# Optimization experiments

Hardware: AMD Instinct MI355X
Metric: run time of the kernel (lower is better)

The kernel has to match this reference:

```python
import jax, jax.numpy as jnp
import numpy as np

B, S, E, H = 2, 2048, 1024, 8
DH = E // H          # v head dim = 128
F = DH // 2          # q/k sub-head dim = 64


def setup_inputs() -> dict:
    key = jax.random.key(0)
    ks = jax.random.split(key, 7)
    sc = E ** -0.5
    return {
        "x": jax.random.normal(ks[0], (B, S, E), dtype=jnp.float32),
        "Wq": jax.random.normal(ks[1], (E, E), dtype=jnp.float32) * sc,
        "Wk": jax.random.normal(ks[2], (E, E), dtype=jnp.float32) * sc,
        "Wv": jax.random.normal(ks[3], (E, E), dtype=jnp.float32) * sc,
        "norm_w": jnp.ones((H, DH), dtype=jnp.float32),
        "Wo": jax.random.normal(ks[4], (E, E), dtype=jnp.float32) * sc,
        "bo": jnp.zeros((E,), dtype=jnp.float32),
        "diff_weight": jnp.float32(0.2),
    }


def reference(x, Wq, Wk, Wv, norm_w, Wo, bo, diff_weight):
    b, s, e = x.shape
    # projections (Linear with weight [out,in] -> x @ W.T)
    qs = (x @ Wq.T).reshape(b, s, H, 2, F)
    ks_ = (x @ Wk.T).reshape(b, s, H, 2, F)
    vs = (x @ Wv.T).reshape(b, s, H, DH)
    scale = F ** -0.5
    # two attention branches: [2, b, h, q, k]
    scores = jnp.einsum('bqhif,bkhif->ibhqk', qs, ks_) * scale
    atts = jax.nn.softmax(scores, axis=-1)
    att = atts[0] - diff_weight * atts[1]          # [b,h,q,k]
    o = jnp.einsum('bhqk,bkhe->bqhe', att, vs)     # [b,q,h,dh]
    # RMSNorm over the joint (heads, head_dim) dims, as in nn.RMSNorm([H, DH])
    eps = jnp.finfo(o.dtype).eps
    rms = jax.lax.rsqrt(jnp.mean(o * o, axis=(-2, -1), keepdims=True) + eps)
    normed = (o * rms * norm_w).reshape(b, s, e)
    return (normed @ Wo.T + bo) * (1.0 - diff_weight)
```

## Files before the change

kernel.cpp:

```cpp
#include <hip/hip_runtime.h>
#include <hip/hip_bf16.h>
#include <math.h>


#define SDIM 2048
#define EDIM 1024
#define HDIM 8
#define DHDIM 128

typedef unsigned short u16;
typedef __attribute__((ext_vector_type(8))) short bf16x8;
typedef __attribute__((ext_vector_type(4))) short bf16x4;
typedef __attribute__((ext_vector_type(4))) u16 u16x4;
typedef __attribute__((ext_vector_type(8))) u16 u16x8;
typedef __attribute__((ext_vector_type(4))) float f32x4;

__device__ __forceinline__ u16 bf16rne(float f) {
    unsigned int u = __float_as_uint(f);
    u += 0x7fff + ((u >> 16) & 1);
    return (u16)(u >> 16);
}

__device__ __forceinline__ void gload16(void* lds, const void* g) {
    __builtin_amdgcn_global_load_lds(
        (const __attribute__((address_space(1))) unsigned int*)g,
        (__attribute__((address_space(3))) unsigned int*)lds, 16, 0, 0);
}

constexpr int GM = 4096, GN = 1024, GK = 1024;

__global__ __launch_bounds__(256) void cast_bf16(
    const float* __restrict__ x,  const float* __restrict__ wq,
    const float* __restrict__ wk, const float* __restrict__ wv,
    const float* __restrict__ wo,
    u16* __restrict__ xb,  u16* __restrict__ wqb, u16* __restrict__ wkb,
    u16* __restrict__ wvb, u16* __restrict__ wob)
{
    int bid = blockIdx.x;
    const float* src; u16* dst; int lb;
    if (bid < 2048)      { src = x;  dst = xb;  lb = bid; }
    else if (bid < 2560) { src = wq; dst = wqb; lb = bid - 2048; }
    else if (bid < 3072) { src = wk; dst = wkb; lb = bid - 2560; }
    else if (bid < 3584) { src = wv; dst = wvb; lb = bid - 3072; }
    else                 { src = wo; dst = wob; lb = bid - 3584; }
    size_t i = ((size_t)lb * 256 + threadIdx.x) * 8;
    float4 a = *(const float4*)&src[i];
    float4 b = *(const float4*)&src[i + 4];
    u16x8 o;
    o[0] = bf16rne(a.x); o[1] = bf16rne(a.y); o[2] = bf16rne(a.z); o[3] = bf16rne(a.w);
    o[4] = bf16rne(b.x); o[5] = bf16rne(b.y); o[6] = bf16rne(b.z); o[7] = bf16rne(b.w);
    *(u16x8*)&dst[i] = o;
}

struct GemmCore {
    f32x4 acc[4][4];
    int m0, n0, wm, wn, ln, quad;
};

__device__ __forceinline__ void gemm_core(
    GemmCore& g, const u16* __restrict__ A, const u16* __restrict__ W,
    u16* AsBase, u16* BsBase)
{
    const int tid = threadIdx.x;
    const int lane = tid & 63;
    const int wv = tid >> 6;
    g.ln = lane & 15; g.quad = lane >> 4;
    g.wm = (wv >> 1) * 64; g.wn = (wv & 1) * 64;
    g.m0 = blockIdx.y * 128; g.n0 = blockIdx.x * 128;

#pragma unroll
    for (int i = 0; i < 4; ++i)
#pragma unroll
        for (int j = 0; j < 4; ++j)
            g.acc[i][j] = (f32x4){0.f, 0.f, 0.f, 0.f};

    const int s0 = tid, s1 = tid + 256, s2 = tid + 512, s3 = tid + 768;
    const int ar0 = s0 >> 3, ac0 = ((s0 & 7) ^ (ar0 & 7)) * 8;
    const int ar1 = s1 >> 3, ac1 = ((s1 & 7) ^ (ar1 & 7)) * 8;
    const int ar2 = s2 >> 3, ac2 = ((s2 & 7) ^ (ar2 & 7)) * 8;
    const int ar3 = s3 >> 3, ac3 = ((s3 & 7) ^ (ar3 & 7)) * 8;
    const u16* pa0 = A + (size_t)(g.m0 + ar0) * GK + ac0;
    const u16* pa1 = A + (size_t)(g.m0 + ar1) * GK + ac1;
    const u16* pa2 = A + (size_t)(g.m0 + ar2) * GK + ac2;
    const u16* pa3 = A + (size_t)(g.m0 + ar3) * GK + ac3;
    const u16* pb0 = W + (size_t)(g.n0 + ar0) * GK + ac0;
    const u16* pb1 = W + (size_t)(g.n0 + ar1) * GK + ac1;
    const u16* pb2 = W + (size_t)(g.n0 + ar2) * GK + ac2;
    const u16* pb3 = W + (size_t)(g.n0 + ar3) * GK + ac3;
    u16* la0 = AsBase + s0 * 8; u16* la1 = AsBase + s1 * 8;
    u16* la2 = AsBase + s2 * 8; u16* la3 = AsBase + s3 * 8;
    u16* lb0 = BsBase + s0 * 8; u16* lb1 = BsBase + s1 * 8;
    u16* lb2 = BsBase + s2 * 8; u16* lb3 = BsBase + s3 * 8;

    for (int k0 = 0; k0 < GK; k0 += 64) {
        gload16(la0, pa0 + k0); gload16(la1, pa1 + k0);
        gload16(la2, pa2 + k0); gload16(la3, pa3 + k0);
        gload16(lb0, pb0 + k0); gload16(lb1, pb1 + k0);
        gload16(lb2, pb2 + k0); gload16(lb3, pb3 + k0);
        __syncthreads();

        bf16x8 af[4][2], bfr[4][2];
#pragma unroll
        for (int t = 0; t < 4; ++t) {
#pragma unroll
            for (int kk = 0; kk < 2; ++kk) {
                const int ra = g.wm + t * 16 + g.ln;
                const int rb = g.wn + t * 16 + g.ln;
                af[t][kk]  = *(const bf16x8*)&AsBase[ra * 64 + (((kk * 4 + g.quad) ^ (ra & 7)) * 8)];
                bfr[t][kk] = *(const bf16x8*)&BsBase[rb * 64 + (((kk * 4 + g.quad) ^ (rb & 7)) * 8)];
            }
        }
#pragma unroll
        for (int i = 0; i < 4; ++i)
#pragma unroll
            for (int j = 0; j < 4; ++j)
#pragma unroll
                for (int kk = 0; kk < 2; ++kk)
                    g.acc[i][j] = __builtin_amdgcn_mfma_f32_16x16x32_bf16(
                        af[i][kk], bfr[j][kk], g.acc[i][j], 0, 0, 0);
        __syncthreads();
    }
}

__global__ __launch_bounds__(256) void gemm_qkv(
    const u16* __restrict__ A,
    const u16* __restrict__ W0, const u16* __restrict__ W1, const u16* __restrict__ W2,
    u16* __restrict__ Qb, u16* __restrict__ Kb, u16* __restrict__ Vtb)
{
    __shared__ u16 As[128 * 64];
    __shared__ u16 Bs[128 * 64];
    const int z = blockIdx.z;
    const u16* W = (z == 0) ? W0 : ((z == 1) ? W1 : W2);
    GemmCore g;
    gemm_core(g, A, W, As, Bs);

    if (z < 2) {
        const float scl = (z == 0) ? 0.125f * 1.44269504f : 1.0f;
        u16* C = (z == 0) ? Qb : Kb;
#pragma unroll
        for (int i = 0; i < 4; ++i) {
            int rb = g.m0 + g.wm + i * 16 + g.quad * 4;
#pragma unroll
            for (int r = 0; r < 4; ++r) {
                u16* crow = C + (size_t)(rb + r) * GN + g.n0 + g.wn + g.ln;
#pragma unroll
                for (int j = 0; j < 4; ++j)
                    crow[j * 16] = bf16rne(g.acc[i][j][r] * scl);
            }
        }
    } else {
        const int bb = g.m0 >> 11;
        const int sb = (g.m0 & 2047) + g.wm + g.quad * 4;
#pragma unroll
        for (int j = 0; j < 4; ++j) {
            int dhg = g.n0 + g.wn + j * 16 + g.ln;
            int hh = dhg >> 7, dh = dhg & 127;
            u16* vrow = Vtb + ((size_t)(bb * 8 + hh) * DHDIM + dh) * SDIM + sb;
#pragma unroll
            for (int i = 0; i < 4; ++i) {
                u16x4 pk;
#pragma unroll
                for (int r = 0; r < 4; ++r) pk[r] = bf16rne(g.acc[i][j][r]);
                *(u16x4*)&vrow[i * 16] = pk;
            }
        }
    }
}

__global__ __launch_bounds__(256) void gemm_out(
    const u16* __restrict__ A, const u16* __restrict__ W,
    float* __restrict__ C, const float* __restrict__ bias,
    const float* __restrict__ dwp)
{
    __shared__ u16 As[128 * 64];
    __shared__ u16 Bs[128 * 64];
    GemmCore g;
    gemm_core(g, A, W, As, Bs);

    const float scale = 1.0f - dwp[0];
    float bv[4];
#pragma unroll
    for (int j = 0; j < 4; ++j) bv[j] = bias[g.n0 + g.wn + j * 16 + g.ln];
#pragma unroll
    for (int i = 0; i < 4; ++i) {
        int rb = g.m0 + g.wm + i * 16 + g.quad * 4;
#pragma unroll
        for (int r = 0; r < 4; ++r) {
            float* crow = C + (size_t)(rb + r) * GN + g.n0 + g.wn + g.ln;
#pragma unroll
            for (int j = 0; j < 4; ++j)
                crow[j * 16] = (g.acc[i][j][r] + bv[j]) * scale;
        }
    }
}

#define KBUF 4096
#define VBUF 8192

__global__ __launch_bounds__(256, 2) void attn_mfma(
    const u16* __restrict__ Qb, const u16* __restrict__ Kb,
    const u16* __restrict__ Vtb,
    float* __restrict__ Oacc, float* __restrict__ Lacc)
{
    __shared__ u16 Ks[2 * KBUF];
    __shared__ u16 Vs[2 * VBUF];

    const int tid = threadIdx.x;
    const int wv   = tid >> 6;
    const int lane = tid & 63;
    const int ln = lane & 15, quad = lane >> 4;
    const int lx = ln & 7;
    const int vkey = (ln >> 1) & 3;
    const int bh = blockIdx.y, b = bh >> 3, h = bh & 7;
    const int q0 = blockIdx.x * 128 + wv * 32;
    const int BR = blockIdx.z;

    const size_t qoff = (size_t)b * SDIM * EDIM + h * DHDIM + BR * 64;
    bf16x8 aq[2][2];
#pragma unroll
    for (int qt = 0; qt < 2; ++qt) {
        const u16* qp = Qb + qoff + (size_t)(q0 + qt * 16 + ln) * EDIM + quad * 8;
        aq[qt][0] = *(const bf16x8*)(qp);
        aq[qt][1] = *(const bf16x8*)(qp + 32);
    }

    const int s0 = tid, s1 = tid + 256;
    const int kr0 = s0 >> 3, kc0 = ((s0 & 7) ^ (kr0 & 7)) * 8;
    const int kr1 = s1 >> 3, kc1 = ((s1 & 7) ^ (kr1 & 7)) * 8;
    const u16* kg0 = Kb + (size_t)(b * SDIM + kr0) * EDIM + h * DHDIM + BR * 64 + kc0;
    const u16* kg1 = Kb + (size_t)(b * SDIM + kr1) * EDIM + h * DHDIM + BR * 64 + kc1;
    const int vr0 = s0 >> 2, vc0 = ((s0 & 3) ^ ((vr0 >> 1) & 3)) * 8;
    const int vr1 = s1 >> 2, vc1 = ((s1 & 3) ^ ((vr1 >> 1) & 3)) * 8;
    const u16* vg0 = Vtb + ((size_t)bh * DHDIM + vr0) * SDIM + vc0;
    const u16* vg1 = Vtb + ((size_t)bh * DHDIM + vr1) * SDIM + vc1;
    u16* ksd0 = Ks + s0 * 8; u16* ksd1 = Ks + s1 * 8;
    u16* vsd0 = Vs + s0 * 8; u16* vsd1 = Vs + s1 * 8;

    gload16(ksd0, kg0); gload16(ksd1, kg1);
    gload16(vsd0, vg0); gload16(vsd1, vg1);
    gload16(vsd0 + 4096, vg0 + 32); gload16(vsd1 + 4096, vg1 + 32);
    kg0 += 64 * EDIM; kg1 += 64 * EDIM; vg0 += 64; vg1 += 64;

    f32x4 acc[2][8];
#pragma unroll
    for (int qt = 0; qt < 2; ++qt)
#pragma unroll
        for (int d = 0; d < 8; ++d)
            acc[qt][d] = (f32x4){0.f, 0.f, 0.f, 0.f};
    float lsum[2] = {0.f, 0.f};
    const f32x4 z4 = (f32x4){0.f, 0.f, 0.f, 0.f};

    for (int it = 0; it < 32; ++it) {
        const int cur = it & 1;
        __syncthreads();

        if (it < 31) {
            const int kb = (cur ^ 1) * KBUF, vb2 = (cur ^ 1) * VBUF;
            gload16(ksd0 + kb, kg0); gload16(ksd1 + kb, kg1);
            gload16(vsd0 + vb2, vg0); gload16(vsd1 + vb2, vg1);
            gload16(vsd0 + vb2 + 4096, vg0 + 32); gload16(vsd1 + vb2 + 4096, vg1 + 32);
            kg0 += 64 * EDIM; kg1 += 64 * EDIM; vg0 += 64; vg1 += 64;
        }

        const u16* Kc = Ks + cur * KBUF;
        const u16* Vc = Vs + cur * VBUF;

        bf16x8 kf[4][2];
#pragma unroll
        for (int t2 = 0; t2 < 4; ++t2) {
            const int rb = (t2 * 16 + ln) * 64;
            kf[t2][0] = *(const bf16x8*)&Kc[rb + ((quad ^ lx) * 8)];
            kf[t2][1] = *(const bf16x8*)&Kc[rb + (((4 + quad) ^ lx) * 8)];
        }

        f32x4 st[2][4];
#pragma unroll
        for (int t2 = 0; t2 < 4; ++t2)
#pragma unroll
            for (int qt = 0; qt < 2; ++qt) {
                f32x4 s = __builtin_amdgcn_mfma_f32_16x16x32_bf16(kf[t2][0], aq[qt][0], z4, 0, 0, 0);
                st[qt][t2] = __builtin_amdgcn_mfma_f32_16x16x32_bf16(kf[t2][1], aq[qt][1], s, 0, 0, 0);
            }

        bf16x8 vf[8][2];
#pragma unroll
        for (int dt = 0; dt < 8; ++dt) {
            const int vb = (dt * 16 + ln) * 32;
#pragma unroll
            for (int ks = 0; ks < 2; ++ks) {
                const u16* Vk = Vc + ks * 4096;
                bf16x4 vlo = *(const bf16x4*)&Vk[vb + ((((quad >> 1) + 0) ^ vkey) * 8 + (quad & 1) * 4)];
                bf16x4 vhi = *(const bf16x4*)&Vk[vb + ((((quad >> 1) + 2) ^ vkey) * 8 + (quad & 1) * 4)];
                vf[dt][ks] = __builtin_shufflevector(vlo, vhi, 0, 1, 2, 3, 4, 5, 6, 7);
            }
        }

        union { unsigned int u[4]; bf16x8 v; } ap[2][2];
#pragma unroll
        for (int qt = 0; qt < 2; ++qt)
#pragma unroll
            for (int ks = 0; ks < 2; ++ks) {
                float e0 = exp2f(st[qt][2 * ks][0]), e1 = exp2f(st[qt][2 * ks][1]);
                float e2 = exp2f(st[qt][2 * ks][2]), e3 = exp2f(st[qt][2 * ks][3]);
                float f0 = exp2f(st[qt][2 * ks + 1][0]), f1 = exp2f(st[qt][2 * ks + 1][1]);
                float f2 = exp2f(st[qt][2 * ks + 1][2]), f3 = exp2f(st[qt][2 * ks + 1][3]);
                lsum[qt] += (e0 + e1) + (e2 + e3) + (f0 + f1) + (f2 + f3);
                ap[qt][ks].u[0] = __builtin_amdgcn_perm(__float_as_uint(e1), __float_as_uint(e0), 0x07060302u);
                ap[qt][ks].u[1] = __builtin_amdgcn_perm(__float_as_uint(e3), __float_as_uint(e2), 0x07060302u);
                ap[qt][ks].u[2] = __builtin_amdgcn_perm(__float_as_uint(f1), __float_as_uint(f0), 0x07060302u);
                ap[qt][ks].u[3] = __builtin_amdgcn_perm(__float_as_uint(f3), __float_as_uint(f2), 0x07060302u);
            }

#pragma unroll
        for (int dt = 0; dt < 8; ++dt)
#pragma unroll
            for (int ks = 0; ks < 2; ++ks)
#pragma unroll
                for (int qt = 0; qt < 2; ++qt)
                    acc[qt][dt] = __builtin_amdgcn_mfma_f32_16x16x32_bf16(ap[qt][ks].v, vf[dt][ks], acc[qt][dt], 0, 0, 0);
    }

#pragma unroll
    for (int qt = 0; qt < 2; ++qt) {
#pragma unroll
        for (int r = 0; r < 4; ++r) {
            size_t row = (size_t)(b * SDIM + q0 + qt * 16 + quad * 4 + r);
            float* o = Oacc + ((row * 8 + h) * 2 + BR) * 128 + ln;
#pragma unroll
            for (int dt = 0; dt < 8; ++dt)
                o[dt * 16] = acc[qt][dt][r];
        }
    }
#pragma unroll
    for (int qt = 0; qt < 2; ++qt) {
        float l = lsum[qt];
        l += __shfl_xor(l, 16, 64); l += __shfl_xor(l, 32, 64);
        if (quad == 0)
            Lacc[(size_t)((b * 8 + h) * 2 + BR) * SDIM + q0 + qt * 16 + ln] = l;
    }
}

__global__ __launch_bounds__(256) void rms_combine(
    const float* __restrict__ Oacc, const float* __restrict__ Lacc,
    const float* __restrict__ nw, u16* __restrict__ Nb,
    const float* __restrict__ dwp)
{
    const int row = blockIdx.x;
    const int tid = threadIdx.x;
    const int h = tid >> 5, dh0 = (tid & 31) * 4;
    const int b = row >> 11, q = row & 2047;

    size_t ob = ((size_t)row * 8 + h) * 2 * 128;
    f32x4 a0 = *(const f32x4*)&Oacc[ob + dh0];
    f32x4 a1 = *(const f32x4*)&Oacc[ob + 128 + dh0];
    float l0 = Lacc[(size_t)((b * 8 + h) * 2 + 0) * SDIM + q];
    float l1 = Lacc[(size_t)((b * 8 + h) * 2 + 1) * SDIM + q];
    const float dw = dwp[0];
    float inv0 = 1.0f / l0;
    float inv1 = dw / l1;
    float o[4];
#pragma unroll
    for (int k = 0; k < 4; ++k) o[k] = a0[k] * inv0 - a1[k] * inv1;

    float ss = o[0] * o[0] + o[1] * o[1] + o[2] * o[2] + o[3] * o[3];
    ss += __shfl_xor(ss, 1,  64);
    ss += __shfl_xor(ss, 2,  64);
    ss += __shfl_xor(ss, 4,  64);
    ss += __shfl_xor(ss, 8,  64);
    ss += __shfl_xor(ss, 16, 64);
    ss += __shfl_xor(ss, 32, 64);
    __shared__ float red[4];
    if ((tid & 63) == 0) red[tid >> 6] = ss;
    __syncthreads();
    float tot = red[0] + red[1] + red[2] + red[3];
    float rms = rsqrtf(tot * (1.0f / 1024.0f) + 1.1920929e-07f);

    float4 w = *(const float4*)&nw[tid * 4];
    u16x4 pk;
    pk[0] = bf16rne(o[0] * rms * w.x);
    pk[1] = bf16rne(o[1] * rms * w.y);
    pk[2] = bf16rne(o[2] * rms * w.z);
    pk[3] = bf16rne(o[3] * rms * w.w);
    *(u16x4*)&Nb[(size_t)row * EDIM + tid * 4] = pk;
}

extern "C" void kernel_launch(void* const* d_in, const int* in_sizes, int n_in,
                              void* d_out, int out_size, void* d_ws, size_t ws_size,
                              hipStream_t stream)
{
    const float* x   = (const float*)d_in[0];
    const float* Wq  = (const float*)d_in[1];
    const float* Wk  = (const float*)d_in[2];
    const float* Wv  = (const float*)d_in[3];
    const float* nw  = (const float*)d_in[4];
    const float* Wo  = (const float*)d_in[5];
    const float* bo  = (const float*)d_in[6];
    const float* dwp = (const float*)d_in[7];
    float* out = (float*)d_out;

    float* Oacc = (float*)d_ws;
    u16*  xb   = (u16*)d_ws;
    u16*  wob  = (u16*)((char*)d_ws + 33554432);
    u16*  wqb  = wob + 1048576;
    u16*  wkb  = wqb + 1048576;
    u16*  wvb  = wkb + 1048576;
    float* Lacc = (float*)wqb;
    u16*  Qb   = wvb + 1048576;
    u16*  Kb   = Qb + 4194304;
    u16*  Vtb  = Kb + 4194304;
    u16*  Nb   = Qb;

    cast_bf16<<<4096, 256, 0, stream>>>(x, Wq, Wk, Wv, Wo,
                                        xb, wqb, wkb, wvb, wob);
    gemm_qkv<<<dim3(GN / 128, GM / 128, 3), 256, 0, stream>>>(
        xb, wqb, wkb, wvb, Qb, Kb, Vtb);
    attn_mfma<<<dim3(SDIM / 128, 2 * HDIM, 2), 256, 0, stream>>>(
        Qb, Kb, Vtb, Oacc, Lacc);
    rms_combine<<<4096, 256, 0, stream>>>(Oacc, Lacc, nw, Nb, dwp);
    gemm_out<<<dim3(GN / 128, GM / 128, 1), 256, 0, stream>>>(
        Nb, wob, out, bo, dwp);
}
```

Baseline: 230.3 us.

## Double-buffer LDS tiles in the GEMM core to overlap loads with MFMA

The shared GEMM core now uses two LDS buffers per operand. It prefetches the next K-tile with global_load_lds while MFMAs run on the current tile, and drops the second barrier per iteration. The goal is to hide global-to-LDS latency in the QKV and output projections. In exchange, LDS use per block doubles to 64 KB, which can lower occupancy.

```diff
diff --git a/kernel.cpp b/kernel.cpp
--- a/kernel.cpp
+++ b/kernel.cpp
@@ -51,6 +51,8 @@
     o[4] = bf16rne(b.x); o[5] = bf16rne(b.y); o[6] = bf16rne(b.z); o[7] = bf16rne(b.w);
     *(u16x8*)&dst[i] = o;
 }
+
+#define GBUF 8192
 
 struct GemmCore {
     f32x4 acc[4][4];
@@ -92,12 +94,25 @@
     u16* lb0 = BsBase + s0 * 8; u16* lb1 = BsBase + s1 * 8;
     u16* lb2 = BsBase + s2 * 8; u16* lb3 = BsBase + s3 * 8;
 
+    gload16(la0, pa0); gload16(la1, pa1);
+    gload16(la2, pa2); gload16(la3, pa3);
+    gload16(lb0, pb0); gload16(lb1, pb1);
+    gload16(lb2, pb2); gload16(lb3, pb3);
+
     for (int k0 = 0; k0 < GK; k0 += 64) {
-        gload16(la0, pa0 + k0); gload16(la1, pa1 + k0);
-        gload16(la2, pa2 + k0); gload16(la3, pa3 + k0);
-        gload16(lb0, pb0 + k0); gload16(lb1, pb1 + k0);
-        gload16(lb2, pb2 + k0); gload16(lb3, pb3 + k0);
+        const int cur = (k0 >> 6) & 1;
         __syncthreads();
+
+        if (k0 + 64 < GK) {
+            const int nb = (cur ^ 1) * GBUF;
+            gload16(la0 + nb, pa0 + k0 + 64); gload16(la1 + nb, pa1 + k0 + 64);
+            gload16(la2 + nb, pa2 + k0 + 64); gload16(la3 + nb, pa3 + k0 + 64);
+            gload16(lb0 + nb, pb0 + k0 + 64); gload16(lb1 + nb, pb1 + k0 + 64);
+            gload16(lb2 + nb, pb2 + k0 + 64); gload16(lb3 + nb, pb3 + k0 + 64);
+        }
+
+        const u16* Ac = AsBase + cur * GBUF;
+        const u16* Bc = BsBase + cur * GBUF;
 
         bf16x8 af[4][2], bfr[4][2];
 #pragma unroll
@@ -106,8 +121,8 @@
             for (int kk = 0; kk < 2; ++kk) {
                 const int ra = g.wm + t * 16 + g.ln;
                 const int rb = g.wn + t * 16 + g.ln;
-                af[t][kk]  = *(const bf16x8*)&AsBase[ra * 64 + (((kk * 4 + g.quad) ^ (ra & 7)) * 8)];
-                bfr[t][kk] = *(const bf16x8*)&BsBase[rb * 64 + (((kk * 4 + g.quad) ^ (rb & 7)) * 8)];
+                af[t][kk]  = *(const bf16x8*)&Ac[ra * 64 + (((kk * 4 + g.quad) ^ (ra & 7)) * 8)];
+                bfr[t][kk] = *(const bf16x8*)&Bc[rb * 64 + (((kk * 4 + g.quad) ^ (rb & 7)) * 8)];
             }
         }
 #pragma unroll
@@ -118,7 +133,6 @@
                 for (int kk = 0; kk < 2; ++kk)
                     g.acc[i][j] = __builtin_amdgcn_mfma_f32_16x16x32_bf16(
                         af[i][kk], bfr[j][kk], g.acc[i][j], 0, 0, 0);
-        __syncthreads();
     }
 }
 
@@ -127,8 +141,8 @@
     const u16* __restrict__ W0, const u16* __restrict__ W1, const u16* __restrict__ W2,
     u16* __restrict__ Qb, u16* __restrict__ Kb, u16* __restrict__ Vtb)
 {
-    __shared__ u16 As[128 * 64];
-    __shared__ u16 Bs[128 * 64];
+    __shared__ u16 As[2 * GBUF];
+    __shared__ u16 Bs[2 * GBUF];
     const int z = blockIdx.z;
     const u16* W = (z == 0) ? W0 : ((z == 1) ? W1 : W2);
     GemmCore g;
@@ -172,8 +186,8 @@
     float* __restrict__ C, const float* __restrict__ bias,
     const float* __restrict__ dwp)
 {
-    __shared__ u16 As[128 * 64];
-    __shared__ u16 Bs[128 * 64];
+    __shared__ u16 As[2 * GBUF];
+    __shared__ u16 Bs[2 * GBUF];
     GemmCore g;
     gemm_core(g, A, W, As, Bs);
 
```

New measurement: 222.2 us. 3.5% less time.
